# Performance work log

Measured on AMD Instinct MI355X. Metric: run time of the kernel, lower is better.

Reference implementation:

```python
import jax, jax.numpy as jnp
import numpy as np


def setup_inputs() -> dict:
    key = jax.random.key(0)
    ks = jax.random.split(key, 9)
    n, L, H, H2 = 1024, 256, 512, 256
    return {
        "lstms0": jax.random.normal(ks[0], (n, L), jnp.float32),
        "lstms1": jax.random.normal(ks[1], (n, L), jnp.float32),
        "W_foh": jax.random.normal(ks[2], (2 * L, H), jnp.float32) * 0.05,
        "W_fom": jax.random.normal(ks[3], (2 * L, H), jnp.float32) * 0.05,
        "catBias": jax.random.normal(ks[4], (1, 2 * H), jnp.float32) * 0.05,
        "hid2Layer": jax.random.normal(ks[5], (2 * H, H2), jnp.float32) * 0.05,
        "hid2Bias": jax.random.normal(ks[6], (1, H2), jnp.float32) * 0.05,
        "outLayer": jax.random.normal(ks[7], (H2, 1), jnp.float32) * 0.05,
        "outBias": jax.random.normal(ks[8], (1, 1), jnp.float32) * 0.05,
    }


def reference(lstms0, lstms1, W_foh, W_fom, catBias, hid2Layer, hid2Bias, outLayer, outBias):
    act = jnp.tanh
    H = W_foh.shape[1]
    # per-token concatenated BiLSTM state: [n, 2L]
    x = jnp.concatenate([lstms0, lstms1], axis=-1)
    headfov = x @ W_foh  # [n, H]
    modfov = x @ W_fom   # [n, H]
    # activation(concat(head_i, mod_j) + catBias) is elementwise, so it splits:
    ah = act(headfov + catBias[0, :H])  # [n, H]
    am = act(modfov + catBias[0, H:])   # [n, H]
    # concat(ah_i, am_j) @ hid2Layer == ah_i @ W_top + am_j @ W_bot
    A = ah @ hid2Layer[:H]  # [n, H2]
    B = am @ hid2Layer[H:]  # [n, H2]
    # pairwise hidden: [n_head, n_mod, H2]
    Z = act(A[:, None, :] + B[None, :, :] + hid2Bias[0])
    scores = jnp.einsum("ijh,h->ij", Z, outLayer[:, 0]) + outBias[0, 0]
    return scores  # [n, n], scores[i, j] = score(head=i, mod=j)
```

## Files before the change

kernel.cpp:

```cpp
#include <hip/hip_runtime.h>
#include <hip/hip_bf16.h>

typedef short s16x4 __attribute__((ext_vector_type(4)));
typedef short s16x8 __attribute__((ext_vector_type(8)));
typedef float f32x4 __attribute__((ext_vector_type(4)));

#define LOG2E_2 2.8853900817779268f

__device__ __forceinline__ float fexp2(float x){ return __builtin_amdgcn_exp2f(x); }
__device__ __forceinline__ float frcp (float x){ return __builtin_amdgcn_rcpf(x); }
__device__ __forceinline__ float ftanh(float v){
    return 1.0f - 2.0f * frcp(1.0f + fexp2(LOG2E_2 * v));
}
__device__ __forceinline__ unsigned short f2bf(float v){
    __hip_bfloat16 h = __float2bfloat16(v);
    return __builtin_bit_cast(unsigned short, h);
}
__device__ __forceinline__ float bf2f(unsigned short u){
    return __bfloat162float(__builtin_bit_cast(__hip_bfloat16, u));
}
__device__ __forceinline__ f32x4 mfma32(s16x8 a, s16x8 b, f32x4 c){
    return __builtin_amdgcn_mfma_f32_16x16x32_bf16(a, b, c, 0, 0, 0);
}

__global__ __launch_bounds__(256) void prep_x(
    const float* __restrict__ l0, const float* __restrict__ l1,
    unsigned short* __restrict__ xhi, unsigned short* __restrict__ xlo)
{
    int idx = (blockIdx.x * 256 + threadIdx.x) * 4;
    int r = idx >> 9, c = idx & 511;
    float4 v = (c < 256) ? *(const float4*)(l0 + r*256 + c)
                         : *(const float4*)(l1 + r*256 + (c - 256));
    ushort4 h, l;
    h.x = f2bf(v.x); l.x = f2bf(v.x - bf2f(h.x));
    h.y = f2bf(v.y); l.y = f2bf(v.y - bf2f(h.y));
    h.z = f2bf(v.z); l.z = f2bf(v.z - bf2f(h.z));
    h.w = f2bf(v.w); l.w = f2bf(v.w - bf2f(h.w));
    *(ushort4*)(xhi + idx) = h;
    *(ushort4*)(xlo + idx) = l;
}

__global__ __launch_bounds__(256) void prep_wt(
    const float* __restrict__ srcA, const float* __restrict__ srcB,
    int splitN, int lda, int K,
    unsigned short* __restrict__ dhi, unsigned short* __restrict__ dlo)
{
    __shared__ float F[32][33];
    const int t = threadIdx.x;
    const int k0 = blockIdx.x * 32, n0 = blockIdx.y * 32;
    {
        int kk = t >> 3, n4 = (t & 7) * 4;
        int n = n0 + n4;
        const float* s = (n < splitN) ? (srcA + (k0+kk)*lda + n)
                                      : (srcB + (k0+kk)*lda + (n - splitN));
        float4 v = *(const float4*)s;
        F[kk][n4+0] = v.x; F[kk][n4+1] = v.y; F[kk][n4+2] = v.z; F[kk][n4+3] = v.w;
    }
    __syncthreads();
    {
        int nn = t >> 3, k4 = (t & 7) * 4;
        ushort4 h, l;
        float v0 = F[k4+0][nn]; h.x = f2bf(v0); l.x = f2bf(v0 - bf2f(h.x));
        float v1 = F[k4+1][nn]; h.y = f2bf(v1); l.y = f2bf(v1 - bf2f(h.y));
        float v2 = F[k4+2][nn]; h.z = f2bf(v2); l.z = f2bf(v2 - bf2f(h.z));
        float v3 = F[k4+3][nn]; h.w = f2bf(v3); l.w = f2bf(v3 - bf2f(h.w));
        *(ushort4*)(dhi + (n0+nn)*K + k0 + k4) = h;
        *(ushort4*)(dlo + (n0+nn)*K + k0 + k4) = l;
    }
}

__global__ __launch_bounds__(256) void k1_mfma(
    const unsigned short* __restrict__ xhi, const unsigned short* __restrict__ xlo,
    const unsigned short* __restrict__ whi, const unsigned short* __restrict__ wlo,
    const float* __restrict__ cb,
    unsigned short* __restrict__ hvhi, unsigned short* __restrict__ hvlo)
{
    __shared__ unsigned short Ah[64][40], Al[64][40], Bh[32][40], Bl[32][40];
    const int t = threadIdx.x;
    const int r0 = blockIdx.y * 64, c0 = blockIdx.x * 32;
    const int w = t >> 6, lane = t & 63;
    const int m = lane & 15, quad = lane >> 4;

    const int arow = t >> 2, aseg = t & 3;
    const int brow = (t & 127) >> 2, bseg = t & 3;
    const bool doB = (t < 128);

    f32x4 acc0 = {0,0,0,0}, acc1 = {0,0,0,0};

    const unsigned short* pAh = xhi + (r0+arow)*512 + aseg*8;
    const unsigned short* pAl = xlo + (r0+arow)*512 + aseg*8;
    const unsigned short* pBh = whi + (c0+brow)*512 + bseg*8;
    const unsigned short* pBl = wlo + (c0+brow)*512 + bseg*8;

    uint4 pah = *(const uint4*)pAh;
    uint4 pal = *(const uint4*)pAl;
    uint4 pbh = {}, pbl = {};
    if (doB) { pbh = *(const uint4*)pBh; pbl = *(const uint4*)pBl; }

    for (int c = 0; c < 16; ++c) {
        __syncthreads();
        *(uint4*)&Ah[arow][aseg*8] = pah;
        *(uint4*)&Al[arow][aseg*8] = pal;
        if (doB) {
            *(uint4*)&Bh[brow][bseg*8] = pbh;
            *(uint4*)&Bl[brow][bseg*8] = pbl;
        }
        __syncthreads();
        if (c + 1 < 16) {
            int k0 = (c+1) * 32;
            pah = *(const uint4*)(pAh + k0);
            pal = *(const uint4*)(pAl + k0);
            if (doB) {
                pbh = *(const uint4*)(pBh + k0);
                pbl = *(const uint4*)(pBl + k0);
            }
        }
        {
            const int ko = quad*8;
            s16x8 ah  = *(const s16x8*)&Ah[w*16 + m][ko];
            s16x8 al  = *(const s16x8*)&Al[w*16 + m][ko];
            s16x8 b0h = *(const s16x8*)&Bh[m][ko];
            s16x8 b0l = *(const s16x8*)&Bl[m][ko];
            s16x8 b1h = *(const s16x8*)&Bh[16 + m][ko];
            s16x8 b1l = *(const s16x8*)&Bl[16 + m][ko];
            acc0 = mfma32(ah, b0h, acc0);
            acc0 = mfma32(ah, b0l, acc0);
            acc0 = mfma32(al, b0h, acc0);
            acc1 = mfma32(ah, b1h, acc1);
            acc1 = mfma32(ah, b1l, acc1);
            acc1 = mfma32(al, b1h, acc1);
        }
    }

    #pragma unroll
    for (int nt = 0; nt < 2; ++nt) {
        f32x4 a = nt ? acc1 : acc0;
        const int col = c0 + nt*16 + m;
        const float bias = cb[col];
        #pragma unroll
        for (int reg = 0; reg < 4; ++reg) {
            const int row = r0 + w*16 + quad*4 + reg;
            float v = ftanh(a[reg] + bias);
            unsigned short h = f2bf(v);
            unsigned short l = f2bf(v - bf2f(h));
            hvhi[row*1024 + col] = h;
            hvlo[row*1024 + col] = l;
        }
    }
}

__global__ __launch_bounds__(256) void k2_mfma(
    const unsigned short* __restrict__ hvhi, const unsigned short* __restrict__ hvlo,
    const unsigned short* __restrict__ w2hi, const unsigned short* __restrict__ w2lo,
    const float* __restrict__ h2b, float* __restrict__ P)
{
    __shared__ unsigned short Ah[64][40], Al[64][40], Bh[32][40], Bl[32][40];
    const int t = threadIdx.x;
    const int r0 = blockIdx.y * 64, c0 = blockIdx.x * 32;
    const int half = (c0 >= 256) ? 1 : 0;
    const int ho = half * 512;
    const int nw = c0 & 255;
    const int w = t >> 6, lane = t & 63;
    const int m = lane & 15, quad = lane >> 4;

    const int arow = t >> 2, aseg = t & 3;
    const int brow = (t & 127) >> 2, bseg = t & 3;
    const bool doB = (t < 128);

    f32x4 acc0 = {0,0,0,0}, acc1 = {0,0,0,0};

    const unsigned short* pAh = hvhi + (r0+arow)*1024 + ho + aseg*8;
    const unsigned short* pAl = hvlo + (r0+arow)*1024 + ho + aseg*8;
    const unsigned short* pBh = w2hi + (nw+brow)*1024 + ho + bseg*8;
    const unsigned short* pBl = w2lo + (nw+brow)*1024 + ho + bseg*8;

    uint4 pah = *(const uint4*)pAh;
    uint4 pal = *(const uint4*)pAl;
    uint4 pbh = {}, pbl = {};
    if (doB) { pbh = *(const uint4*)pBh; pbl = *(const uint4*)pBl; }

    for (int c = 0; c < 16; ++c) {
        __syncthreads();
        *(uint4*)&Ah[arow][aseg*8] = pah;
        *(uint4*)&Al[arow][aseg*8] = pal;
        if (doB) {
            *(uint4*)&Bh[brow][bseg*8] = pbh;
            *(uint4*)&Bl[brow][bseg*8] = pbl;
        }
        __syncthreads();
        if (c + 1 < 16) {
            int k0 = (c+1) * 32;
            pah = *(const uint4*)(pAh + k0);
            pal = *(const uint4*)(pAl + k0);
            if (doB) {
                pbh = *(const uint4*)(pBh + k0);
                pbl = *(const uint4*)(pBl + k0);
            }
        }
        {
            const int ko = quad*8;
            s16x8 ah  = *(const s16x8*)&Ah[w*16 + m][ko];
            s16x8 al  = *(const s16x8*)&Al[w*16 + m][ko];
            s16x8 b0h = *(const s16x8*)&Bh[m][ko];
            s16x8 b0l = *(const s16x8*)&Bl[m][ko];
            s16x8 b1h = *(const s16x8*)&Bh[16 + m][ko];
            s16x8 b1l = *(const s16x8*)&Bl[16 + m][ko];
            acc0 = mfma32(ah, b0h, acc0);
            acc0 = mfma32(ah, b0l, acc0);
            acc0 = mfma32(al, b0h, acc0);
            acc1 = mfma32(ah, b1h, acc1);
            acc1 = mfma32(ah, b1l, acc1);
            acc1 = mfma32(al, b1h, acc1);
        }
    }

    #pragma unroll
    for (int nt = 0; nt < 2; ++nt) {
        f32x4 a = nt ? acc1 : acc0;
        const int col = c0 + nt*16 + m;
        const float bias = half ? 0.0f : h2b[col];
        #pragma unroll
        for (int reg = 0; reg < 4; ++reg) {
            const int row = r0 + w*16 + quad*4 + reg;
            P[row*512 + col] = fexp2((a[reg] + bias) * LOG2E_2);
        }
    }
}

__global__ __launch_bounds__(256) void k3_pairwise(
    const float* __restrict__ P, const float* __restrict__ w,
    const float* __restrict__ ob, float* __restrict__ out)
{
    __shared__ float As[32][68];
    __shared__ float Bs[64][34];
    __shared__ float wls[256];
    const int tid = threadIdx.x;
    const int tx = tid & 15;
    const int ty = tid >> 4;
    const int i0 = blockIdx.y * 32, j0 = blockIdx.x * 32;

    wls[tid] = w[tid];

    int rr0 = tid >> 4,        c40 = (tid & 15) * 4;
    int rr1 = (tid + 256) >> 4, c41 = (tid & 15) * 4;

    float acc[2][2] = {};

    float4 pa0 = *(const float4*)&P[(i0+rr0)*512 + 0 + c40];
    float4 pa1 = *(const float4*)&P[(i0+rr1)*512 + 0 + c41];
    float4 pb0 = *(const float4*)&P[(j0+rr0)*512 + 256 + 0 + c40];
    float4 pb1 = *(const float4*)&P[(j0+rr1)*512 + 256 + 0 + c41];

    for (int c = 0; c < 4; ++c) {
        __syncthreads();
        *(float4*)&As[rr0][c40] = pa0;
        *(float4*)&As[rr1][c41] = pa1;
        Bs[c40+0][rr0] = pb0.x; Bs[c40+1][rr0] = pb0.y;
        Bs[c40+2][rr0] = pb0.z; Bs[c40+3][rr0] = pb0.w;
        Bs[c41+0][rr1] = pb1.x; Bs[c41+1][rr1] = pb1.y;
        Bs[c41+2][rr1] = pb1.z; Bs[c41+3][rr1] = pb1.w;
        __syncthreads();
        if (c + 1 < 4) {
            int h0 = (c+1) * 64;
            pa0 = *(const float4*)&P[(i0+rr0)*512 + h0 + c40];
            pa1 = *(const float4*)&P[(i0+rr1)*512 + h0 + c41];
            pb0 = *(const float4*)&P[(j0+rr0)*512 + 256 + h0 + c40];
            pb1 = *(const float4*)&P[(j0+rr1)*512 + 256 + h0 + c41];
        }

        for (int hh = 0; hh < 64; hh += 4) {
            float4 wv = *(const float4*)&wls[c*64 + hh];
            float4 a0 = *(const float4*)&As[ty*2+0][hh];
            float4 a1 = *(const float4*)&As[ty*2+1][hh];
            float2 b0 = *(const float2*)&Bs[hh+0][tx*2];
            float2 b1 = *(const float2*)&Bs[hh+1][tx*2];
            float2 b2 = *(const float2*)&Bs[hh+2][tx*2];
            float2 b3 = *(const float2*)&Bs[hh+3][tx*2];
            float aa[2][4] = {{a0.x,a0.y,a0.z,a0.w},{a1.x,a1.y,a1.z,a1.w}};
            float bb[4][2] = {{b0.x,b0.y},{b1.x,b1.y},{b2.x,b2.y},{b3.x,b3.y}};
            float ww[4] = {wv.x, wv.y, wv.z, wv.w};
            #pragma unroll
            for (int h = 0; h < 4; ++h)
                #pragma unroll
                for (int r = 0; r < 2; ++r)
                    #pragma unroll
                    for (int q = 0; q < 2; ++q) {
                        float u = fmaf(aa[r][h], bb[h][q], 1.0f);
                        acc[r][q] = fmaf(ww[h], frcp(u), acc[r][q]);
                    }
        }
    }

    float sumw = 0.0f;
    #pragma unroll
    for (int h = 0; h < 256; h += 4) {
        float4 wv = *(const float4*)&wls[h];
        sumw += (wv.x + wv.y) + (wv.z + wv.w);
    }
    const float base = ob[0] + sumw;
    const int row = i0 + ty*2;
    const int col = j0 + tx*2;
    #pragma unroll
    for (int r = 0; r < 2; ++r) {
        float2 o;
        o.x = base - 2.0f*acc[r][0];
        o.y = base - 2.0f*acc[r][1];
        *(float2*)&out[(row+r)*1024 + col] = o;
    }
}

extern "C" void kernel_launch(void* const* d_in, const int* in_sizes, int n_in,
                              void* d_out, int out_size, void* d_ws, size_t ws_size,
                              hipStream_t stream) {
    const float* l0   = (const float*)d_in[0];
    const float* l1   = (const float*)d_in[1];
    const float* Wfoh = (const float*)d_in[2];
    const float* Wfom = (const float*)d_in[3];
    const float* cb   = (const float*)d_in[4];
    const float* W2   = (const float*)d_in[5];
    const float* h2b  = (const float*)d_in[6];
    const float* w    = (const float*)d_in[7];
    const float* ob   = (const float*)d_in[8];
    float* out = (float*)d_out;

    unsigned short* hv_hi  = (unsigned short*)d_ws;
    unsigned short* hv_lo  = hv_hi + 1024*1024;
    float*          P      = (float*)(hv_lo + 1024*1024);
    unsigned short* xs_hi  = (unsigned short*)(P + 1024*512);
    unsigned short* xs_lo  = xs_hi + 1024*512;
    unsigned short* w1t_hi = xs_lo + 1024*512;
    unsigned short* w1t_lo = w1t_hi + 1024*512;
    unsigned short* w2t_hi = w1t_lo + 1024*512;
    unsigned short* w2t_lo = w2t_hi + 256*1024;

    prep_x<<<512, 256, 0, stream>>>(l0, l1, xs_hi, xs_lo);
    prep_wt<<<dim3(16,32), 256, 0, stream>>>(Wfoh, Wfom, 512, 512, 512, w1t_hi, w1t_lo);
    prep_wt<<<dim3(32,8),  256, 0, stream>>>(W2, W2, 1<<30, 256, 1024, w2t_hi, w2t_lo);
    k1_mfma<<<dim3(32,16), 256, 0, stream>>>(xs_hi, xs_lo, w1t_hi, w1t_lo, cb, hv_hi, hv_lo);
    k2_mfma<<<dim3(16,16), 256, 0, stream>>>(hv_hi, hv_lo, w2t_hi, w2t_lo, h2b, P);
    k3_pairwise<<<dim3(32,32), 256, 0, stream>>>(P, w, ob, out);
}
```

Before: 131.0 us.

## Merge prep kernels and double-buffer GEMM stages with 512-thread blocks

Combines the three input/weight preparation kernels into a single launch dispatched by block index. The two MFMA GEMM kernels move to 512-thread blocks with double-buffered shared-memory tiles, a two-stage register prefetch and a single barrier per k-step. The hidden activation hi/lo bf16 pair is packed into one 32-bit word so k2 reads it with a single load stream. This aims to cut launch overhead and barrier stalls, at the cost of more shared memory per block and more complex staging logic.

```diff
diff --git a/kernel.cpp b/kernel.cpp
--- a/kernel.cpp
+++ b/kernel.cpp
@@ -1,7 +1,6 @@
 #include <hip/hip_runtime.h>
 #include <hip/hip_bf16.h>
 
-typedef short s16x4 __attribute__((ext_vector_type(4)));
 typedef short s16x8 __attribute__((ext_vector_type(8)));
 typedef float f32x4 __attribute__((ext_vector_type(4)));
 
@@ -23,31 +22,46 @@
     return __builtin_amdgcn_mfma_f32_16x16x32_bf16(a, b, c, 0, 0, 0);
 }
 
-__global__ __launch_bounds__(256) void prep_x(
+__global__ __launch_bounds__(256) void prep_all(
     const float* __restrict__ l0, const float* __restrict__ l1,
-    unsigned short* __restrict__ xhi, unsigned short* __restrict__ xlo)
+    const float* __restrict__ Wfoh, const float* __restrict__ Wfom,
+    const float* __restrict__ W2,
+    unsigned short* __restrict__ xs_hi, unsigned short* __restrict__ xs_lo,
+    unsigned short* __restrict__ w1t_hi, unsigned short* __restrict__ w1t_lo,
+    unsigned short* __restrict__ w2t_hi, unsigned short* __restrict__ w2t_lo)
 {
-    int idx = (blockIdx.x * 256 + threadIdx.x) * 4;
-    int r = idx >> 9, c = idx & 511;
-    float4 v = (c < 256) ? *(const float4*)(l0 + r*256 + c)
-                         : *(const float4*)(l1 + r*256 + (c - 256));
-    ushort4 h, l;
-    h.x = f2bf(v.x); l.x = f2bf(v.x - bf2f(h.x));
-    h.y = f2bf(v.y); l.y = f2bf(v.y - bf2f(h.y));
-    h.z = f2bf(v.z); l.z = f2bf(v.z - bf2f(h.z));
-    h.w = f2bf(v.w); l.w = f2bf(v.w - bf2f(h.w));
-    *(ushort4*)(xhi + idx) = h;
-    *(ushort4*)(xlo + idx) = l;
-}
-
-__global__ __launch_bounds__(256) void prep_wt(
-    const float* __restrict__ srcA, const float* __restrict__ srcB,
-    int splitN, int lda, int K,
-    unsigned short* __restrict__ dhi, unsigned short* __restrict__ dlo)
-{
+    const int b = blockIdx.x;
+    const int t = threadIdx.x;
+    if (b < 512) {
+        int idx = (b*256 + t) * 4;
+        int r = idx >> 9, c = idx & 511;
+        float4 v = (c < 256) ? *(const float4*)(l0 + r*256 + c)
+                             : *(const float4*)(l1 + r*256 + (c - 256));
+        ushort4 h, l;
+        h.x = f2bf(v.x); l.x = f2bf(v.x - bf2f(h.x));
+        h.y = f2bf(v.y); l.y = f2bf(v.y - bf2f(h.y));
+        h.z = f2bf(v.z); l.z = f2bf(v.z - bf2f(h.z));
+        h.w = f2bf(v.w); l.w = f2bf(v.w - bf2f(h.w));
+        *(ushort4*)(xs_hi + idx) = h;
+        *(ushort4*)(xs_lo + idx) = l;
+        return;
+    }
     __shared__ float F[32][33];
-    const int t = threadIdx.x;
-    const int k0 = blockIdx.x * 32, n0 = blockIdx.y * 32;
+    int k0, n0, K;
+    const float *srcA, *srcB;
+    int splitN, lda;
+    unsigned short *dhi, *dlo;
+    if (b < 1024) {
+        int tb = b - 512;
+        k0 = (tb & 15) * 32; n0 = (tb >> 4) * 32; K = 512;
+        srcA = Wfoh; srcB = Wfom; splitN = 512; lda = 512;
+        dhi = w1t_hi; dlo = w1t_lo;
+    } else {
+        int tb = b - 1024;
+        k0 = (tb & 31) * 32; n0 = (tb >> 5) * 32; K = 1024;
+        srcA = W2; srcB = W2; splitN = 1 << 30; lda = 256;
+        dhi = w2t_hi; dlo = w2t_lo;
+    }
     {
         int kk = t >> 3, n4 = (t & 7) * 4;
         int n = n0 + n4;
@@ -69,60 +83,49 @@
     }
 }
 
-__global__ __launch_bounds__(256) void k1_mfma(
-    const unsigned short* __restrict__ xhi, const unsigned short* __restrict__ xlo,
-    const unsigned short* __restrict__ whi, const unsigned short* __restrict__ wlo,
-    const float* __restrict__ cb,
-    unsigned short* __restrict__ hvhi, unsigned short* __restrict__ hvlo)
+__global__ __launch_bounds__(512) void k1_mfma(
+    const unsigned short* __restrict__ xs_hi, const unsigned short* __restrict__ xs_lo,
+    const unsigned short* __restrict__ w1t_hi, const unsigned short* __restrict__ w1t_lo,
+    const float* __restrict__ cb, unsigned int* __restrict__ hv)
 {
-    __shared__ unsigned short Ah[64][40], Al[64][40], Bh[32][40], Bl[32][40];
+    __shared__ unsigned short Ah[2][64][40], Al[2][64][40], Bh[2][64][40], Bl[2][64][40];
     const int t = threadIdx.x;
-    const int r0 = blockIdx.y * 64, c0 = blockIdx.x * 32;
+    const int bx = blockIdx.x & 15, by = blockIdx.x >> 4;
+    const int r0 = by*64, c0 = bx*64;
     const int w = t >> 6, lane = t & 63;
     const int m = lane & 15, quad = lane >> 4;
-
-    const int arow = t >> 2, aseg = t & 3;
-    const int brow = (t & 127) >> 2, bseg = t & 3;
-    const bool doB = (t < 128);
+    const int ms = (w & 3)*16, ns = (w >> 2)*32;
+
+    const int srow = (t & 255) >> 2;
+    const int sk   = (t & 3) * 8;
+    const bool isA = (t < 256);
+    const unsigned short* ghi = isA ? (xs_hi + (r0+srow)*512 + sk) : (w1t_hi + (c0+srow)*512 + sk);
+    const unsigned short* glo = isA ? (xs_lo + (r0+srow)*512 + sk) : (w1t_lo + (c0+srow)*512 + sk);
+
+    uint4 rh[2], rl[2];
+    rh[0] = *(const uint4*)(ghi);      rl[0] = *(const uint4*)(glo);
+    rh[1] = *(const uint4*)(ghi + 32); rl[1] = *(const uint4*)(glo + 32);
+
+    if (isA) { *(uint4*)&Ah[0][srow][sk] = rh[0]; *(uint4*)&Al[0][srow][sk] = rl[0]; }
+    else     { *(uint4*)&Bh[0][srow][sk] = rh[0]; *(uint4*)&Bl[0][srow][sk] = rl[0]; }
+    __syncthreads();
 
     f32x4 acc0 = {0,0,0,0}, acc1 = {0,0,0,0};
 
-    const unsigned short* pAh = xhi + (r0+arow)*512 + aseg*8;
-    const unsigned short* pAl = xlo + (r0+arow)*512 + aseg*8;
-    const unsigned short* pBh = whi + (c0+brow)*512 + bseg*8;
-    const unsigned short* pBl = wlo + (c0+brow)*512 + bseg*8;
-
-    uint4 pah = *(const uint4*)pAh;
-    uint4 pal = *(const uint4*)pAl;
-    uint4 pbh = {}, pbl = {};
-    if (doB) { pbh = *(const uint4*)pBh; pbl = *(const uint4*)pBl; }
-
     for (int c = 0; c < 16; ++c) {
-        __syncthreads();
-        *(uint4*)&Ah[arow][aseg*8] = pah;
-        *(uint4*)&Al[arow][aseg*8] = pal;
-        if (doB) {
-            *(uint4*)&Bh[brow][bseg*8] = pbh;
-            *(uint4*)&Bl[brow][bseg*8] = pbl;
-        }
-        __syncthreads();
-        if (c + 1 < 16) {
-            int k0 = (c+1) * 32;
-            pah = *(const uint4*)(pAh + k0);
-            pal = *(const uint4*)(pAl + k0);
-            if (doB) {
-                pbh = *(const uint4*)(pBh + k0);
-                pbl = *(const uint4*)(pBl + k0);
-            }
+        const int s0 = c & 1, s1 = (c+1) & 1;
+        if (c + 2 < 16) {
+            rh[s0] = *(const uint4*)(ghi + (c+2)*32);
+            rl[s0] = *(const uint4*)(glo + (c+2)*32);
         }
         {
             const int ko = quad*8;
-            s16x8 ah  = *(const s16x8*)&Ah[w*16 + m][ko];
-            s16x8 al  = *(const s16x8*)&Al[w*16 + m][ko];
-            s16x8 b0h = *(const s16x8*)&Bh[m][ko];
-            s16x8 b0l = *(const s16x8*)&Bl[m][ko];
-            s16x8 b1h = *(const s16x8*)&Bh[16 + m][ko];
-            s16x8 b1l = *(const s16x8*)&Bl[16 + m][ko];
+            s16x8 ah  = *(const s16x8*)&Ah[s0][ms+m][ko];
+            s16x8 al  = *(const s16x8*)&Al[s0][ms+m][ko];
+            s16x8 b0h = *(const s16x8*)&Bh[s0][ns+m][ko];
+            s16x8 b0l = *(const s16x8*)&Bl[s0][ns+m][ko];
+            s16x8 b1h = *(const s16x8*)&Bh[s0][ns+16+m][ko];
+            s16x8 b1l = *(const s16x8*)&Bl[s0][ns+16+m][ko];
             acc0 = mfma32(ah, b0h, acc0);
             acc0 = mfma32(ah, b0l, acc0);
             acc0 = mfma32(al, b0h, acc0);
@@ -130,100 +133,105 @@
             acc1 = mfma32(ah, b1l, acc1);
             acc1 = mfma32(al, b1h, acc1);
         }
+        if (c + 1 < 16) {
+            if (isA) { *(uint4*)&Ah[s1][srow][sk] = rh[s1]; *(uint4*)&Al[s1][srow][sk] = rl[s1]; }
+            else     { *(uint4*)&Bh[s1][srow][sk] = rh[s1]; *(uint4*)&Bl[s1][srow][sk] = rl[s1]; }
+            __syncthreads();
+        }
     }
 
     #pragma unroll
     for (int nt = 0; nt < 2; ++nt) {
         f32x4 a = nt ? acc1 : acc0;
-        const int col = c0 + nt*16 + m;
+        const int col = c0 + ns + nt*16 + m;
         const float bias = cb[col];
         #pragma unroll
         for (int reg = 0; reg < 4; ++reg) {
-            const int row = r0 + w*16 + quad*4 + reg;
+            const int row = r0 + ms + quad*4 + reg;
             float v = ftanh(a[reg] + bias);
             unsigned short h = f2bf(v);
             unsigned short l = f2bf(v - bf2f(h));
-            hvhi[row*1024 + col] = h;
-            hvlo[row*1024 + col] = l;
-        }
-    }
-}
-
-__global__ __launch_bounds__(256) void k2_mfma(
-    const unsigned short* __restrict__ hvhi, const unsigned short* __restrict__ hvlo,
-    const unsigned short* __restrict__ w2hi, const unsigned short* __restrict__ w2lo,
+            hv[row*1024 + col] = (unsigned int)h | ((unsigned int)l << 16);
+        }
+    }
+}
+
+__global__ __launch_bounds__(512) void k2_mfma(
+    const unsigned int* __restrict__ hv,
+    const unsigned short* __restrict__ w2t_hi, const unsigned short* __restrict__ w2t_lo,
     const float* __restrict__ h2b, float* __restrict__ P)
 {
-    __shared__ unsigned short Ah[64][40], Al[64][40], Bh[32][40], Bl[32][40];
+    __shared__ unsigned short Ah[2][64][40], Al[2][64][40], Bh[2][32][40], Bl[2][32][40];
     const int t = threadIdx.x;
-    const int r0 = blockIdx.y * 64, c0 = blockIdx.x * 32;
+    const int bx = blockIdx.x & 15, by = blockIdx.x >> 4;
+    const int r0 = by*64, c0 = bx*32;
     const int half = (c0 >= 256) ? 1 : 0;
     const int ho = half * 512;
     const int nw = c0 & 255;
     const int w = t >> 6, lane = t & 63;
     const int m = lane & 15, quad = lane >> 4;
-
-    const int arow = t >> 2, aseg = t & 3;
-    const int brow = (t & 127) >> 2, bseg = t & 3;
-    const bool doB = (t < 128);
-
-    f32x4 acc0 = {0,0,0,0}, acc1 = {0,0,0,0};
-
-    const unsigned short* pAh = hvhi + (r0+arow)*1024 + ho + aseg*8;
-    const unsigned short* pAl = hvlo + (r0+arow)*1024 + ho + aseg*8;
-    const unsigned short* pBh = w2hi + (nw+brow)*1024 + ho + bseg*8;
-    const unsigned short* pBl = w2lo + (nw+brow)*1024 + ho + bseg*8;
-
-    uint4 pah = *(const uint4*)pAh;
-    uint4 pal = *(const uint4*)pAl;
-    uint4 pbh = {}, pbl = {};
-    if (doB) { pbh = *(const uint4*)pBh; pbl = *(const uint4*)pBl; }
+    const int ms = (w & 3)*16, ns = (w >> 2)*16;
+
+    const int arow = t >> 3, akk = (t & 7) * 4;
+    const int brow = (t & 127) >> 2, bkk = (t & 3) * 8;
+    const bool doBh = (t < 128), doBl = (t >= 128 && t < 256);
+
+    const unsigned int*   gA  = hv + (r0+arow)*1024 + ho + akk;
+    const unsigned short* gBh = w2t_hi + (nw+brow)*1024 + ho + bkk;
+    const unsigned short* gBl = w2t_lo + (nw+brow)*1024 + ho + bkk;
+
+    uint4 ra[2], rb[2];
+    ra[0] = *(const uint4*)(gA);
+    ra[1] = *(const uint4*)(gA + 32);
+    rb[0] = doBh ? *(const uint4*)(gBh) : (doBl ? *(const uint4*)(gBl) : make_uint4(0,0,0,0));
+    rb[1] = doBh ? *(const uint4*)(gBh + 32) : (doBl ? *(const uint4*)(gBl + 32) : make_uint4(0,0,0,0));
+
+    f32x4 acc = {0,0,0,0};
+
+    {
+        ushort4 h = make_ushort4(ra[0].x & 0xffff, ra[0].y & 0xffff, ra[0].z & 0xffff, ra[0].w & 0xffff);
+        ushort4 l = make_ushort4(ra[0].x >> 16,    ra[0].y >> 16,    ra[0].z >> 16,    ra[0].w >> 16);
+        *(ushort4*)&Ah[0][arow][akk] = h;
+        *(ushort4*)&Al[0][arow][akk] = l;
+        if (doBh) *(uint4*)&Bh[0][brow][bkk] = rb[0];
+        if (doBl) *(uint4*)&Bl[0][brow][bkk] = rb[0];
+    }
+    __syncthreads();
 
     for (int c = 0; c < 16; ++c) {
-        __syncthreads();
-        *(uint4*)&Ah[arow][aseg*8] = pah;
-        *(uint4*)&Al[arow][aseg*8] = pal;
-        if (doB) {
-            *(uint4*)&Bh[brow][bseg*8] = pbh;
-            *(uint4*)&Bl[brow][bseg*8] = pbl;
-        }
-        __syncthreads();
-        if (c + 1 < 16) {
-            int k0 = (c+1) * 32;
-            pah = *(const uint4*)(pAh + k0);
-            pal = *(const uint4*)(pAl + k0);
-            if (doB) {
-                pbh = *(const uint4*)(pBh + k0);
-                pbl = *(const uint4*)(pBl + k0);
-            }
+        const int s0 = c & 1, s1 = (c+1) & 1;
+        if (c + 2 < 16) {
+            ra[s0] = *(const uint4*)(gA + (c+2)*32);
+            if (doBh) rb[s0] = *(const uint4*)(gBh + (c+2)*32);
+            if (doBl) rb[s0] = *(const uint4*)(gBl + (c+2)*32);
         }
         {
             const int ko = quad*8;
-            s16x8 ah  = *(const s16x8*)&Ah[w*16 + m][ko];
-            s16x8 al  = *(const s16x8*)&Al[w*16 + m][ko];
-            s16x8 b0h = *(const s16x8*)&Bh[m][ko];
-            s16x8 b0l = *(const s16x8*)&Bl[m][ko];
-            s16x8 b1h = *(const s16x8*)&Bh[16 + m][ko];
-            s16x8 b1l = *(const s16x8*)&Bl[16 + m][ko];
-            acc0 = mfma32(ah, b0h, acc0);
-            acc0 = mfma32(ah, b0l, acc0);
-            acc0 = mfma32(al, b0h, acc0);
-            acc1 = mfma32(ah, b1h, acc1);
-            acc1 = mfma32(ah, b1l, acc1);
-            acc1 = mfma32(al, b1h, acc1);
-        }
-    }
-
+            s16x8 ah = *(const s16x8*)&Ah[s0][ms+m][ko];
+            s16x8 al = *(const s16x8*)&Al[s0][ms+m][ko];
+            s16x8 bh = *(const s16x8*)&Bh[s0][ns+m][ko];
+            s16x8 bl = *(const s16x8*)&Bl[s0][ns+m][ko];
+            acc = mfma32(ah, bh, acc);
+            acc = mfma32(ah, bl, acc);
+            acc = mfma32(al, bh, acc);
+        }
+        if (c + 1 < 16) {
+            ushort4 h = make_ushort4(ra[s1].x & 0xffff, ra[s1].y & 0xffff, ra[s1].z & 0xffff, ra[s1].w & 0xffff);
+            ushort4 l = make_ushort4(ra[s1].x >> 16,    ra[s1].y >> 16,    ra[s1].z >> 16,    ra[s1].w >> 16);
+            *(ushort4*)&Ah[s1][arow][akk] = h;
+            *(ushort4*)&Al[s1][arow][akk] = l;
+            if (doBh) *(uint4*)&Bh[s1][brow][bkk] = rb[s1];
+            if (doBl) *(uint4*)&Bl[s1][brow][bkk] = rb[s1];
+            __syncthreads();
+        }
+    }
+
+    const int col = c0 + ns + m;
+    const float bias = half ? 0.0f : h2b[col];
     #pragma unroll
-    for (int nt = 0; nt < 2; ++nt) {
-        f32x4 a = nt ? acc1 : acc0;
-        const int col = c0 + nt*16 + m;
-        const float bias = half ? 0.0f : h2b[col];
-        #pragma unroll
-        for (int reg = 0; reg < 4; ++reg) {
-            const int row = r0 + w*16 + quad*4 + reg;
-            P[row*512 + col] = fexp2((a[reg] + bias) * LOG2E_2);
-        }
+    for (int reg = 0; reg < 4; ++reg) {
+        const int row = r0 + ms + quad*4 + reg;
+        P[row*512 + col] = fexp2((acc[reg] + bias) * LOG2E_2);
     }
 }
 
@@ -241,7 +249,7 @@
 
     wls[tid] = w[tid];
 
-    int rr0 = tid >> 4,        c40 = (tid & 15) * 4;
+    int rr0 = tid >> 4,         c40 = (tid & 15) * 4;
     int rr1 = (tid + 256) >> 4, c41 = (tid & 15) * 4;
 
     float acc[2][2] = {};
@@ -323,20 +331,18 @@
     const float* ob   = (const float*)d_in[8];
     float* out = (float*)d_out;
 
-    unsigned short* hv_hi  = (unsigned short*)d_ws;
-    unsigned short* hv_lo  = hv_hi + 1024*1024;
-    float*          P      = (float*)(hv_lo + 1024*1024);
+    unsigned int*   hv     = (unsigned int*)d_ws;
+    float*          P      = (float*)(hv + 1024*1024);
     unsigned short* xs_hi  = (unsigned short*)(P + 1024*512);
-    unsigned short* xs_lo  = xs_hi + 1024*512;
-    unsigned short* w1t_hi = xs_lo + 1024*512;
+    unsigned short* xs_lo  = xs_hi  + 1024*512;
+    unsigned short* w1t_hi = xs_lo  + 1024*512;
     unsigned short* w1t_lo = w1t_hi + 1024*512;
     unsigned short* w2t_hi = w1t_lo + 1024*512;
     unsigned short* w2t_lo = w2t_hi + 256*1024;
 
-    prep_x<<<512, 256, 0, stream>>>(l0, l1, xs_hi, xs_lo);
-    prep_wt<<<dim3(16,32), 256, 0, stream>>>(Wfoh, Wfom, 512, 512, 512, w1t_hi, w1t_lo);
-    prep_wt<<<dim3(32,8),  256, 0, stream>>>(W2, W2, 1<<30, 256, 1024, w2t_hi, w2t_lo);
-    k1_mfma<<<dim3(32,16), 256, 0, stream>>>(xs_hi, xs_lo, w1t_hi, w1t_lo, cb, hv_hi, hv_lo);
-    k2_mfma<<<dim3(16,16), 256, 0, stream>>>(hv_hi, hv_lo, w2t_hi, w2t_lo, h2b, P);
+    prep_all<<<1280, 256, 0, stream>>>(l0, l1, Wfoh, Wfom, W2,
+                                       xs_hi, xs_lo, w1t_hi, w1t_lo, w2t_hi, w2t_lo);
+    k1_mfma<<<256, 512, 0, stream>>>(xs_hi, xs_lo, w1t_hi, w1t_lo, cb, hv);
+    k2_mfma<<<256, 512, 0, stream>>>(hv, w2t_hi, w2t_lo, h2b, P);
     k3_pairwise<<<dim3(32,32), 256, 0, stream>>>(P, w, ob, out);
 }
```

After: 138.9 us. 6.1% more time.
